# Kernel optimization log

Measured on AMD Instinct MI355X. Metric: run time of the kernel, lower is better.

## Reference

```python
import jax, jax.numpy as jnp
import numpy as np

M, N, D_MODEL = 16, 2048, 512
H, D = 8, 64  # num_heads, head_dim; inner_dim = H*D = 512


def setup_inputs() -> dict:
    key = jax.random.key(0)
    ks = jax.random.split(key, 8)
    s = 1.0 / np.sqrt(D_MODEL)
    return {
        "xq": jax.random.normal(ks[0], (M, N, D_MODEL), jnp.float32),
        "xk": jax.random.normal(ks[1], (M, N, D_MODEL), jnp.float32),
        "xv": jax.random.normal(ks[2], (M, N, D_MODEL), jnp.float32),
        "Wq": jax.random.normal(ks[3], (D_MODEL, H * D), jnp.float32) * s,
        "Wk": jax.random.normal(ks[4], (D_MODEL, H * D), jnp.float32) * s,
        "Wv": jax.random.normal(ks[5], (D_MODEL, H * D), jnp.float32) * s,
        "Wo": jax.random.normal(ks[6], (H * D, D_MODEL), jnp.float32) * s,
        "bo": jnp.zeros((D_MODEL,), jnp.float32),
    }


def _split_heads(x):
    # [m, n, h*d] -> [m, h, n, d]
    m, n, _ = x.shape
    return x.reshape(m, n, H, D).transpose(0, 2, 1, 3)


def reference(xq, xk, xv, Wq, Wk, Wv, Wo, bo):
    scale = D ** -0.5
    q = _split_heads(xq @ Wq)
    k = _split_heads(xk @ Wk)
    v = _split_heads(xv @ Wv)
    # linear attention: softmax over feature dim for both q and k
    q = jax.nn.softmax(q, axis=-1) * scale
    k = jax.nn.softmax(k, axis=-1)
    kv = jnp.einsum('mhnd,mhne->mhde', k, v)   # [m, h, d, d]
    out = jnp.einsum('mhqd,mhde->mhqe', q, kv)  # [m, h, nq, d]
    out = out.transpose(0, 2, 1, 3).reshape(out.shape[0], -1, H * D)
    return out @ Wo + bo
```

## Files before the change

kernel.cpp:

```cpp
#include <hip/hip_runtime.h>
#include <hip/hip_bf16.h>


typedef __bf16 bf16;
typedef __bf16 bf16x8 __attribute__((ext_vector_type(8)));
typedef __bf16 bf16x4 __attribute__((ext_vector_type(4)));
typedef float  f32x4  __attribute__((ext_vector_type(4)));

#define MFMA16(a, b, c) __builtin_amdgcn_mfma_f32_16x16x32_bf16((a), (b), (c), 0, 0, 0)

__device__ inline bf16x8 cvt8(float4 a, float4 b) {
  bf16x8 h;
  h[0] = (bf16)a.x; h[1] = (bf16)a.y; h[2] = (bf16)a.z; h[3] = (bf16)a.w;
  h[4] = (bf16)b.x; h[5] = (bf16)b.y; h[6] = (bf16)b.z; h[7] = (bf16)b.w;
  return h;
}

__global__ __launch_bounds__(256) void k_prep_frag(const float* __restrict__ w0, const float* __restrict__ w1,
                                                   const float* __restrict__ w2,
                                                   bf16* __restrict__ f0, bf16* __restrict__ f1,
                                                   bf16* __restrict__ f2)
{
  const float* W = (blockIdx.z == 0) ? w0 : (blockIdx.z == 1) ? w1 : w2;
  bf16*        F = (blockIdx.z == 0) ? f0 : (blockIdx.z == 1) ? f1 : f2;
  __shared__ float lds[64][68];
  const int t = threadIdx.x;
  const int bx = blockIdx.x, by = blockIdx.y;
  {
    const int r = t >> 2, c0 = (t & 3) << 4;
    const float* src = W + (size_t)(bx * 64 + r) * 512 + by * 64 + c0;
    float4 a = ((const float4*)src)[0], b = ((const float4*)src)[1];
    float4 c = ((const float4*)src)[2], d = ((const float4*)src)[3];
    *(float4*)&lds[r][c0 + 0]  = a; *(float4*)&lds[r][c0 + 4]  = b;
    *(float4*)&lds[r][c0 + 8]  = c; *(float4*)&lds[r][c0 + 12] = d;
  }
  __syncthreads();
#pragma unroll
  for (int it = 0; it < 2; ++it) {
    const int ch = t + it * 256;
    const int kc = ch >> 6, cc = ch & 63;
    bf16x8 v;
#pragma unroll
    for (int j = 0; j < 8; ++j) v[j] = (bf16)lds[kc * 8 + j][cc];
    const int cg   = by >> 1;
    const int cb7  = ((by & 1) << 2) | (cc >> 4);
    const int ksub = kc >> 2, g = kc & 3, li = cc & 15;
    const size_t off = (size_t)cg * 65536 + (size_t)bx * 8192 + ksub * 4096 + cb7 * 512 + (g * 16 + li) * 8;
    *(bf16x8*)(F + off) = v;
  }
}

__global__ __launch_bounds__(256) void k_prep_wo(const float* __restrict__ W, bf16* __restrict__ T)
{
  __shared__ float lds[64][68];
  const int t = threadIdx.x;
  const int r = t >> 2, c0 = (t & 3) << 4;
  const float* src = W + (size_t)(blockIdx.x * 64 + r) * 512 + blockIdx.y * 64 + c0;
  float4 f0 = ((const float4*)src)[0];
  float4 f1 = ((const float4*)src)[1];
  float4 f2 = ((const float4*)src)[2];
  float4 f3 = ((const float4*)src)[3];
  *(float4*)&lds[r][c0 + 0]  = f0;
  *(float4*)&lds[r][c0 + 4]  = f1;
  *(float4*)&lds[r][c0 + 8]  = f2;
  *(float4*)&lds[r][c0 + 12] = f3;
  __syncthreads();
  bf16 v[16];
#pragma unroll
  for (int s = 0; s < 16; ++s) v[s] = (bf16)lds[c0 + s][r];
  bf16* dst = T + (size_t)(blockIdx.y * 64 + r) * 512 + blockIdx.x * 64 + c0;
  *(bf16x8*)&dst[0] = *(bf16x8*)&v[0];
  *(bf16x8*)&dst[8] = *(bf16x8*)&v[8];
}

__global__ __launch_bounds__(512, 2) void k_qkv(const float* __restrict__ xq, const float* __restrict__ xk,
                                                const float* __restrict__ xv,
                                                const bf16* __restrict__ Fq, const bf16* __restrict__ Fk,
                                                const bf16* __restrict__ Fv,
                                                bf16* __restrict__ Qo, bf16* __restrict__ Ko,
                                                bf16* __restrict__ Vo)
{
  const int proj = blockIdx.z;
  const float* X  = (proj == 0) ? xq : (proj == 1) ? xk : xv;
  const bf16*  F  = (proj == 0) ? Fq : (proj == 1) ? Fk : Fv;
  bf16*       OUT = (proj == 0) ? Qo : (proj == 1) ? Ko : Vo;

  __shared__ bf16 As[2][128][72];

  const int t = threadIdx.x, lane = t & 63, w = t >> 6;
  const int g = lane >> 4, li = lane & 15;
  const size_t arow = (size_t)blockIdx.x * 128;

  const bf16* Fw = F + (w >> 1) * 65536 + (w & 1) * 2048 + lane * 8;

  const int sr = t >> 2, sc = (t & 3) << 4;
  const float* xp0 = X + (arow + sr) * 512 + sc;

  f32x4 acc[8][4] = {};

  {
    float4 xa[4];
#pragma unroll
    for (int i = 0; i < 4; ++i) xa[i] = ((const float4*)xp0)[i];
    *(bf16x8*)&As[0][sr][sc]     = cvt8(xa[0], xa[1]);
    *(bf16x8*)&As[0][sr][sc + 8] = cvt8(xa[2], xa[3]);
  }
  bf16x8 bfc[4];
#pragma unroll
  for (int ct = 0; ct < 4; ++ct) bfc[ct] = *(const bf16x8*)(Fw + ct * 512);
  __syncthreads();

  float4 xa[4];
#pragma unroll
  for (int hs = 0; hs < 16; ++hs) {
    const int kt = hs >> 1, cur = kt & 1;
    bf16x8 bfn[4];
    if (hs < 15) {
      const bf16* p = Fw + ((hs + 1) >> 1) * 8192 + ((hs + 1) & 1) * 4096;
#pragma unroll
      for (int ct = 0; ct < 4; ++ct) bfn[ct] = *(const bf16x8*)(p + ct * 512);
    }
    if ((hs & 1) == 0 && kt < 7) {
#pragma unroll
      for (int i = 0; i < 4; ++i) xa[i] = ((const float4*)(xp0 + (kt + 1) * 64))[i];
    }
    {
      bf16x8 af[8];
#pragma unroll
      for (int rt = 0; rt < 8; ++rt)
        af[rt] = *(const bf16x8*)&As[cur][rt * 16 + li][(hs & 1) * 32 + g * 8];
#pragma unroll
      for (int rt = 0; rt < 8; ++rt)
#pragma unroll
        for (int ct = 0; ct < 4; ++ct)
          acc[rt][ct] = MFMA16(af[rt], bfc[ct], acc[rt][ct]);
    }
    if (hs & 1) {
      if (kt < 7) {
        *(bf16x8*)&As[cur ^ 1][sr][sc]     = cvt8(xa[0], xa[1]);
        *(bf16x8*)&As[cur ^ 1][sr][sc + 8] = cvt8(xa[2], xa[3]);
      }
      if (hs < 15) __syncthreads();
    }
    if (hs < 15) {
#pragma unroll
      for (int ct = 0; ct < 4; ++ct) bfc[ct] = bfn[ct];
    }
  }

#pragma unroll
  for (int rt = 0; rt < 8; ++rt) {
#pragma unroll
    for (int q = 0; q < 4; ++q) {
      float v0 = acc[rt][0][q], v1 = acc[rt][1][q], v2 = acc[rt][2][q], v3 = acc[rt][3][q];
      if (proj < 2) {
        float mx = fmaxf(fmaxf(v0, v1), fmaxf(v2, v3));
        mx = fmaxf(mx, __shfl_xor(mx, 1));
        mx = fmaxf(mx, __shfl_xor(mx, 2));
        mx = fmaxf(mx, __shfl_xor(mx, 4));
        mx = fmaxf(mx, __shfl_xor(mx, 8));
        v0 = __expf(v0 - mx); v1 = __expf(v1 - mx); v2 = __expf(v2 - mx); v3 = __expf(v3 - mx);
        float s = v0 + v1 + v2 + v3;
        s += __shfl_xor(s, 1); s += __shfl_xor(s, 2); s += __shfl_xor(s, 4); s += __shfl_xor(s, 8);
        const float inv = (proj == 0 ? 0.125f : 1.0f) / s;
        v0 *= inv; v1 *= inv; v2 *= inv; v3 *= inv;
      }
      bf16* o = OUT + (arow + rt * 16 + g * 4 + q) * 512 + w * 64 + li;
      o[0] = (bf16)v0; o[16] = (bf16)v1; o[32] = (bf16)v2; o[48] = (bf16)v3;
    }
  }
}

__global__ __launch_bounds__(256) void k_kv(const bf16* __restrict__ K, const bf16* __restrict__ V,
                                            float* __restrict__ kvp)
{
  const int mh = blockIdx.x, m = mh >> 3, h = mh & 7;
  const int ns = blockIdx.y;
  __shared__ bf16 Kt[64][40];
  __shared__ bf16 Vt[64][40];
  const int t = threadIdx.x, lane = t & 63, wave = t >> 6;
  const int dq = wave >> 1, eq = wave & 1;
  const int g = lane >> 4, li = lane & 15;
  const int tn = t & 31, d0 = (t >> 5) << 3;
  const size_t rowbase = (size_t)m * 2048 + ns * 512;

  f32x4 acc[2][2] = {};

  for (int nt = 0; nt < 16; ++nt) {
    __syncthreads();
    {
      bf16x8 kr = *(const bf16x8*)(K + (rowbase + nt * 32 + tn) * 512 + h * 64 + d0);
      bf16x8 vr = *(const bf16x8*)(V + (rowbase + nt * 32 + tn) * 512 + h * 64 + d0);
#pragma unroll
      for (int j = 0; j < 8; ++j) Kt[d0 + j][tn] = kr[j];
#pragma unroll
      for (int j = 0; j < 8; ++j) Vt[d0 + j][tn] = vr[j];
    }
    __syncthreads();
    bf16x8 af[2], bfr[2];
#pragma unroll
    for (int dt = 0; dt < 2; ++dt) af[dt]  = *(const bf16x8*)&Kt[dq * 32 + dt * 16 + li][g * 8];
#pragma unroll
    for (int et = 0; et < 2; ++et) bfr[et] = *(const bf16x8*)&Vt[eq * 32 + et * 16 + li][g * 8];
#pragma unroll
    for (int dt = 0; dt < 2; ++dt)
#pragma unroll
      for (int et = 0; et < 2; ++et)
        acc[dt][et] = MFMA16(af[dt], bfr[et], acc[dt][et]);
  }

  float* o = kvp + ((size_t)mh * 4 + ns) * 4096;
#pragma unroll
  for (int dt = 0; dt < 2; ++dt)
#pragma unroll
    for (int et = 0; et < 2; ++et)
#pragma unroll
      for (int q = 0; q < 4; ++q) {
        const int d = dq * 32 + dt * 16 + g * 4 + q;
        const int e = eq * 32 + et * 16 + li;
        o[d * 64 + e] = acc[dt][et][q];
      }
}

__global__ __launch_bounds__(512) void k_wfused(const float* __restrict__ kvp, const bf16* __restrict__ WoT,
                                                bf16* __restrict__ WfT)
{
  const int mh = blockIdx.x, m = mh >> 3, h = mh & 7;
  __shared__ bf16 kvs[64][72];
  const int t = threadIdx.x, lane = t & 63, wave = t >> 6;
  const int g = lane >> 4, li = lane & 15;
  {
    const int d = t >> 3, e0 = (t & 7) << 3;
    const float* p = kvp + (size_t)mh * 16384 + d * 64 + e0;
#pragma unroll
    for (int j = 0; j < 8; ++j) {
      float s = p[j] + p[4096 + j] + p[8192 + j] + p[12288 + j];
      kvs[d][e0 + j] = (bf16)s;
    }
  }
  __syncthreads();
  f32x4 acc[4][4] = {};
#pragma unroll
  for (int kk = 0; kk < 2; ++kk) {
    bf16x8 af[4], bfr[4];
#pragma unroll
    for (int rt = 0; rt < 4; ++rt) {
      const int c = wave * 64 + rt * 16 + li;
      af[rt] = *(const bf16x8*)(WoT + (size_t)c * 512 + h * 64 + kk * 32 + g * 8);
    }
#pragma unroll
    for (int ct = 0; ct < 4; ++ct)
      bfr[ct] = *(const bf16x8*)&kvs[ct * 16 + li][kk * 32 + g * 8];
#pragma unroll
    for (int rt = 0; rt < 4; ++rt)
#pragma unroll
      for (int ct = 0; ct < 4; ++ct)
        acc[rt][ct] = MFMA16(af[rt], bfr[ct], acc[rt][ct]);
  }
  bf16* o = WfT + (size_t)m * 262144;
#pragma unroll
  for (int rt = 0; rt < 4; ++rt)
#pragma unroll
    for (int ct = 0; ct < 4; ++ct)
#pragma unroll
      for (int q = 0; q < 4; ++q) {
        const int c = wave * 64 + rt * 16 + g * 4 + q;
        const int r = h * 64 + ct * 16 + li;
        o[(size_t)c * 512 + r] = (bf16)acc[rt][ct][q];
      }
}

__global__ __launch_bounds__(512) void k_out(const bf16* __restrict__ Q, const bf16* __restrict__ WfT,
                                             const float* __restrict__ bo, float* __restrict__ out)
{
  __shared__ bf16 As2[64][40];
  __shared__ bf16 Bs[512][40];
  const int rb = blockIdx.x;
  const int m = rb >> 5;
  const bf16* B = WfT + (size_t)m * 262144;
  const int t = threadIdx.x, lane = t & 63, wave = t >> 6;
  const int g = lane >> 4, li = lane & 15;
  const size_t arow = (size_t)rb * 64;

  f32x4 acc[4][4] = {};
  const int ar = t >> 3, ac = (t & 7) << 2;
  const int br = t >> 2, bc = (t & 3) << 3;

  for (int kt = 0; kt < 16; ++kt) {
    const int k0 = kt * 32;
    __syncthreads();
    {
      bf16x4 a = *(const bf16x4*)(Q + (arow + ar) * 512 + k0 + ac);
      *(bf16x4*)&As2[ar][ac] = a;
    }
#pragma unroll
    for (int i = 0; i < 4; ++i) {
      const int r = br + i * 128;
      bf16x8 b = *(const bf16x8*)(B + (size_t)r * 512 + k0 + bc);
      *(bf16x8*)&Bs[r][bc] = b;
    }
    __syncthreads();
    bf16x8 af[4], bfr[4];
#pragma unroll
    for (int rt = 0; rt < 4; ++rt) af[rt]  = *(const bf16x8*)&As2[rt * 16 + li][g * 8];
#pragma unroll
    for (int ct = 0; ct < 4; ++ct) bfr[ct] = *(const bf16x8*)&Bs[wave * 64 + ct * 16 + li][g * 8];
#pragma unroll
    for (int rt = 0; rt < 4; ++rt)
#pragma unroll
      for (int ct = 0; ct < 4; ++ct)
        acc[rt][ct] = MFMA16(af[rt], bfr[ct], acc[rt][ct]);
  }

  float bv[4];
#pragma unroll
  for (int ct = 0; ct < 4; ++ct) bv[ct] = bo[wave * 64 + ct * 16 + li];
#pragma unroll
  for (int rt = 0; rt < 4; ++rt)
#pragma unroll
    for (int q = 0; q < 4; ++q) {
      float* o = out + (arow + rt * 16 + g * 4 + q) * 512 + wave * 64 + li;
      o[0]  = acc[rt][0][q] + bv[0];
      o[16] = acc[rt][1][q] + bv[1];
      o[32] = acc[rt][2][q] + bv[2];
      o[48] = acc[rt][3][q] + bv[3];
    }
}

extern "C" void kernel_launch(void* const* d_in, const int* in_sizes, int n_in,
                              void* d_out, int out_size, void* d_ws, size_t ws_size,
                              hipStream_t stream)
{
  const float* xq = (const float*)d_in[0];
  const float* xk = (const float*)d_in[1];
  const float* xv = (const float*)d_in[2];
  const float* Wq = (const float*)d_in[3];
  const float* Wk = (const float*)d_in[4];
  const float* Wv = (const float*)d_in[5];
  const float* Wo = (const float*)d_in[6];
  const float* bo = (const float*)d_in[7];
  float* out = (float*)d_out;

  char* ws = (char*)d_ws;
  const size_t WT_BYTES  = 512 * 512 * 2;
  const size_t QKV_BYTES = (size_t)32768 * 512 * 2;
  bf16*  WFq = (bf16*)(ws);
  bf16*  WFk = (bf16*)(ws + WT_BYTES);
  bf16*  WFv = (bf16*)(ws + 2 * WT_BYTES);
  bf16*  WoT = (bf16*)(ws + 3 * WT_BYTES);
  bf16*  Qb  = (bf16*)(ws + 4 * WT_BYTES);
  bf16*  Kb  = (bf16*)(ws + 4 * WT_BYTES + QKV_BYTES);
  bf16*  Vb  = (bf16*)(ws + 4 * WT_BYTES + 2 * QKV_BYTES);
  float* kvp = (float*)(ws + 4 * WT_BYTES + 3 * QKV_BYTES);
  bf16*  WfT = Kb;

  k_prep_frag<<<dim3(8, 8, 3), 256, 0, stream>>>(Wq, Wk, Wv, WFq, WFk, WFv);
  k_prep_wo  <<<dim3(8, 8),    256, 0, stream>>>(Wo, WoT);
  k_qkv      <<<dim3(256, 1, 3), 512, 0, stream>>>(xq, xk, xv, WFq, WFk, WFv, Qb, Kb, Vb);
  k_kv       <<<dim3(128, 4),  256, 0, stream>>>(Kb, Vb, kvp);
  k_wfused   <<<dim3(128),     512, 0, stream>>>(kvp, WoT, WfT);
  k_out      <<<dim3(512),     512, 0, stream>>>(Qb, WfT, bo, out);
}
```

Measured before the change: 178.2 us.

## Drop LDS staging in QKV and output GEMMs, read MFMA fragments directly

The QKV projection kernel now uses 64-row tiles with a flat 1536-block grid and no LDS double buffering. Each lane loads and converts its A fragment straight from global fp32 memory, and occupancy is raised to 4 blocks per CU. The fused-weight kernel now writes its output in a pre-swizzled MFMA fragment layout, so the output GEMM can load B fragments directly from global memory without LDS or barriers. This removes shared-memory traffic and syncs but gives up cross-wave reuse of A tiles, which means more redundant global and L2 reads.

```diff
diff --git a/kernel.cpp b/kernel.cpp
--- a/kernel.cpp
+++ b/kernel.cpp
@@ -73,83 +73,51 @@
   *(bf16x8*)&dst[8] = *(bf16x8*)&v[8];
 }
 
-__global__ __launch_bounds__(512, 2) void k_qkv(const float* __restrict__ xq, const float* __restrict__ xk,
+__global__ __launch_bounds__(512, 4) void k_qkv(const float* __restrict__ xq, const float* __restrict__ xk,
                                                 const float* __restrict__ xv,
                                                 const bf16* __restrict__ Fq, const bf16* __restrict__ Fk,
                                                 const bf16* __restrict__ Fv,
                                                 bf16* __restrict__ Qo, bf16* __restrict__ Ko,
                                                 bf16* __restrict__ Vo)
 {
-  const int proj = blockIdx.z;
+  const int b = blockIdx.x;
+  const int proj = b >> 9;
+  const int rb   = b & 511;
   const float* X  = (proj == 0) ? xq : (proj == 1) ? xk : xv;
   const bf16*  F  = (proj == 0) ? Fq : (proj == 1) ? Fk : Fv;
   bf16*       OUT = (proj == 0) ? Qo : (proj == 1) ? Ko : Vo;
 
-  __shared__ bf16 As[2][128][72];
-
   const int t = threadIdx.x, lane = t & 63, w = t >> 6;
   const int g = lane >> 4, li = lane & 15;
-  const size_t arow = (size_t)blockIdx.x * 128;
-
-  const bf16* Fw = F + (w >> 1) * 65536 + (w & 1) * 2048 + lane * 8;
-
-  const int sr = t >> 2, sc = (t & 3) << 4;
-  const float* xp0 = X + (arow + sr) * 512 + sc;
-
-  f32x4 acc[8][4] = {};
-
-  {
-    float4 xa[4];
-#pragma unroll
-    for (int i = 0; i < 4; ++i) xa[i] = ((const float4*)xp0)[i];
-    *(bf16x8*)&As[0][sr][sc]     = cvt8(xa[0], xa[1]);
-    *(bf16x8*)&As[0][sr][sc + 8] = cvt8(xa[2], xa[3]);
-  }
-  bf16x8 bfc[4];
-#pragma unroll
-  for (int ct = 0; ct < 4; ++ct) bfc[ct] = *(const bf16x8*)(Fw + ct * 512);
-  __syncthreads();
-
-  float4 xa[4];
-#pragma unroll
-  for (int hs = 0; hs < 16; ++hs) {
-    const int kt = hs >> 1, cur = kt & 1;
-    bf16x8 bfn[4];
-    if (hs < 15) {
-      const bf16* p = Fw + ((hs + 1) >> 1) * 8192 + ((hs + 1) & 1) * 4096;
-#pragma unroll
-      for (int ct = 0; ct < 4; ++ct) bfn[ct] = *(const bf16x8*)(p + ct * 512);
-    }
-    if ((hs & 1) == 0 && kt < 7) {
-#pragma unroll
-      for (int i = 0; i < 4; ++i) xa[i] = ((const float4*)(xp0 + (kt + 1) * 64))[i];
-    }
-    {
-      bf16x8 af[8];
-#pragma unroll
-      for (int rt = 0; rt < 8; ++rt)
-        af[rt] = *(const bf16x8*)&As[cur][rt * 16 + li][(hs & 1) * 32 + g * 8];
-#pragma unroll
-      for (int rt = 0; rt < 8; ++rt)
-#pragma unroll
-        for (int ct = 0; ct < 4; ++ct)
-          acc[rt][ct] = MFMA16(af[rt], bfc[ct], acc[rt][ct]);
-    }
-    if (hs & 1) {
-      if (kt < 7) {
-        *(bf16x8*)&As[cur ^ 1][sr][sc]     = cvt8(xa[0], xa[1]);
-        *(bf16x8*)&As[cur ^ 1][sr][sc + 8] = cvt8(xa[2], xa[3]);
-      }
-      if (hs < 15) __syncthreads();
-    }
-    if (hs < 15) {
-#pragma unroll
-      for (int ct = 0; ct < 4; ++ct) bfc[ct] = bfn[ct];
-    }
-  }
-
-#pragma unroll
-  for (int rt = 0; rt < 8; ++rt) {
+  const size_t arow = (size_t)rb * 64;
+
+  const float* ap = X + (arow + li) * 512 + g * 8;
+  const bf16*  bp = F + (w >> 1) * 65536 + (w & 1) * 2048 + lane * 8;
+
+  f32x4 acc[4][4] = {};
+
+#pragma unroll 4
+  for (int kt = 0; kt < 16; ++kt) {
+    bf16x8 af[4], bfr[4];
+#pragma unroll
+    for (int rt = 0; rt < 4; ++rt) {
+      const float* p = ap + rt * 8192 + kt * 32;
+      float4 f0 = ((const float4*)p)[0];
+      float4 f1 = ((const float4*)p)[1];
+      af[rt] = cvt8(f0, f1);
+    }
+#pragma unroll
+    for (int ct = 0; ct < 4; ++ct)
+      bfr[ct] = *(const bf16x8*)(bp + kt * 4096 + ct * 512);
+#pragma unroll
+    for (int rt = 0; rt < 4; ++rt)
+#pragma unroll
+      for (int ct = 0; ct < 4; ++ct)
+        acc[rt][ct] = MFMA16(af[rt], bfr[ct], acc[rt][ct]);
+  }
+
+#pragma unroll
+  for (int rt = 0; rt < 4; ++rt) {
 #pragma unroll
     for (int q = 0; q < 4; ++q) {
       float v0 = acc[rt][0][q], v1 = acc[rt][1][q], v2 = acc[rt][2][q], v3 = acc[rt][3][q];
@@ -223,11 +191,11 @@
 }
 
 __global__ __launch_bounds__(512) void k_wfused(const float* __restrict__ kvp, const bf16* __restrict__ WoT,
-                                                bf16* __restrict__ WfT)
+                                                bf16* __restrict__ WfF)
 {
   const int mh = blockIdx.x, m = mh >> 3, h = mh & 7;
   __shared__ bf16 kvs[64][72];
-  const int t = threadIdx.x, lane = t & 63, wave = t >> 6;
+  const int t = threadIdx.x, lane = t & 63, wv = t >> 6;
   const int g = lane >> 4, li = lane & 15;
   {
     const int d = t >> 3, e0 = (t & 7) << 3;
@@ -242,84 +210,77 @@
   f32x4 acc[4][4] = {};
 #pragma unroll
   for (int kk = 0; kk < 2; ++kk) {
+    bf16x8 a_kv[4], b_wo[4];
+#pragma unroll
+    for (int rt = 0; rt < 4; ++rt)
+      a_kv[rt] = *(const bf16x8*)&kvs[rt * 16 + li][kk * 32 + g * 8];
+#pragma unroll
+    for (int ct = 0; ct < 4; ++ct) {
+      const int cout = wv * 64 + ct * 16 + li;
+      b_wo[ct] = *(const bf16x8*)(WoT + (size_t)cout * 512 + h * 64 + kk * 32 + g * 8);
+    }
+#pragma unroll
+    for (int rt = 0; rt < 4; ++rt)
+#pragma unroll
+      for (int ct = 0; ct < 4; ++ct)
+        acc[rt][ct] = MFMA16(a_kv[rt], b_wo[ct], acc[rt][ct]);
+  }
+  bf16* o = WfF + (size_t)m * 262144;
+#pragma unroll
+  for (int rt = 0; rt < 4; ++rt)
+#pragma unroll
+    for (int ct = 0; ct < 4; ++ct) {
+      const int cgct  = wv * 4 + ct;
+      const int cg    = cgct >> 3, cb7 = cgct & 7;
+      const int lane2 = ((rt & 1) * 2 + (g >> 1)) * 16 + li;
+      const size_t off = (size_t)cg * 65536 + (size_t)h * 8192 + (rt >> 1) * 4096
+                       + cb7 * 512 + lane2 * 8 + (g & 1) * 4;
+      bf16x4 v;
+#pragma unroll
+      for (int q = 0; q < 4; ++q) v[q] = (bf16)acc[rt][ct][q];
+      *(bf16x4*)(o + off) = v;
+    }
+}
+
+__global__ __launch_bounds__(512, 4) void k_out(const bf16* __restrict__ Q, const bf16* __restrict__ WfF,
+                                                const float* __restrict__ bo, float* __restrict__ out)
+{
+  const int rb = blockIdx.x;
+  const int m  = rb >> 5;
+  const bf16* Fm = WfF + (size_t)m * 262144;
+  const int t = threadIdx.x, lane = t & 63, w = t >> 6;
+  const int g = lane >> 4, li = lane & 15;
+  const size_t arow = (size_t)rb * 64;
+
+  const bf16* apq = Q + (arow + li) * 512 + g * 8;
+  const bf16* bp  = Fm + (w >> 1) * 65536 + (w & 1) * 2048 + lane * 8;
+
+  f32x4 acc[4][4] = {};
+
+#pragma unroll 4
+  for (int kt = 0; kt < 16; ++kt) {
     bf16x8 af[4], bfr[4];
 #pragma unroll
-    for (int rt = 0; rt < 4; ++rt) {
-      const int c = wave * 64 + rt * 16 + li;
-      af[rt] = *(const bf16x8*)(WoT + (size_t)c * 512 + h * 64 + kk * 32 + g * 8);
-    }
+    for (int rt = 0; rt < 4; ++rt)
+      af[rt] = *(const bf16x8*)(apq + rt * 8192 + kt * 32);
 #pragma unroll
     for (int ct = 0; ct < 4; ++ct)
-      bfr[ct] = *(const bf16x8*)&kvs[ct * 16 + li][kk * 32 + g * 8];
+      bfr[ct] = *(const bf16x8*)(bp + kt * 4096 + ct * 512);
 #pragma unroll
     for (int rt = 0; rt < 4; ++rt)
 #pragma unroll
       for (int ct = 0; ct < 4; ++ct)
         acc[rt][ct] = MFMA16(af[rt], bfr[ct], acc[rt][ct]);
   }
-  bf16* o = WfT + (size_t)m * 262144;
+
+  float bv[4];
+#pragma unroll
+  for (int ct = 0; ct < 4; ++ct) bv[ct] = bo[w * 64 + ct * 16 + li];
 #pragma unroll
   for (int rt = 0; rt < 4; ++rt)
 #pragma unroll
-    for (int ct = 0; ct < 4; ++ct)
-#pragma unroll
-      for (int q = 0; q < 4; ++q) {
-        const int c = wave * 64 + rt * 16 + g * 4 + q;
-        const int r = h * 64 + ct * 16 + li;
-        o[(size_t)c * 512 + r] = (bf16)acc[rt][ct][q];
-      }
-}
-
-__global__ __launch_bounds__(512) void k_out(const bf16* __restrict__ Q, const bf16* __restrict__ WfT,
-                                             const float* __restrict__ bo, float* __restrict__ out)
-{
-  __shared__ bf16 As2[64][40];
-  __shared__ bf16 Bs[512][40];
-  const int rb = blockIdx.x;
-  const int m = rb >> 5;
-  const bf16* B = WfT + (size_t)m * 262144;
-  const int t = threadIdx.x, lane = t & 63, wave = t >> 6;
-  const int g = lane >> 4, li = lane & 15;
-  const size_t arow = (size_t)rb * 64;
-
-  f32x4 acc[4][4] = {};
-  const int ar = t >> 3, ac = (t & 7) << 2;
-  const int br = t >> 2, bc = (t & 3) << 3;
-
-  for (int kt = 0; kt < 16; ++kt) {
-    const int k0 = kt * 32;
-    __syncthreads();
-    {
-      bf16x4 a = *(const bf16x4*)(Q + (arow + ar) * 512 + k0 + ac);
-      *(bf16x4*)&As2[ar][ac] = a;
-    }
-#pragma unroll
-    for (int i = 0; i < 4; ++i) {
-      const int r = br + i * 128;
-      bf16x8 b = *(const bf16x8*)(B + (size_t)r * 512 + k0 + bc);
-      *(bf16x8*)&Bs[r][bc] = b;
-    }
-    __syncthreads();
-    bf16x8 af[4], bfr[4];
-#pragma unroll
-    for (int rt = 0; rt < 4; ++rt) af[rt]  = *(const bf16x8*)&As2[rt * 16 + li][g * 8];
-#pragma unroll
-    for (int ct = 0; ct < 4; ++ct) bfr[ct] = *(const bf16x8*)&Bs[wave * 64 + ct * 16 + li][g * 8];
-#pragma unroll
-    for (int rt = 0; rt < 4; ++rt)
-#pragma unroll
-      for (int ct = 0; ct < 4; ++ct)
-        acc[rt][ct] = MFMA16(af[rt], bfr[ct], acc[rt][ct]);
-  }
-
-  float bv[4];
-#pragma unroll
-  for (int ct = 0; ct < 4; ++ct) bv[ct] = bo[wave * 64 + ct * 16 + li];
-#pragma unroll
-  for (int rt = 0; rt < 4; ++rt)
-#pragma unroll
     for (int q = 0; q < 4; ++q) {
-      float* o = out + (arow + rt * 16 + g * 4 + q) * 512 + wave * 64 + li;
+      float* o = out + (arow + rt * 16 + g * 4 + q) * 512 + w * 64 + li;
       o[0]  = acc[rt][0][q] + bv[0];
       o[16] = acc[rt][1][q] + bv[1];
       o[32] = acc[rt][2][q] + bv[2];
@@ -352,12 +313,12 @@
   bf16*  Kb  = (bf16*)(ws + 4 * WT_BYTES + QKV_BYTES);
   bf16*  Vb  = (bf16*)(ws + 4 * WT_BYTES + 2 * QKV_BYTES);
   float* kvp = (float*)(ws + 4 * WT_BYTES + 3 * QKV_BYTES);
-  bf16*  WfT = Kb;
+  bf16*  WfF = Kb;
 
   k_prep_frag<<<dim3(8, 8, 3), 256, 0, stream>>>(Wq, Wk, Wv, WFq, WFk, WFv);
   k_prep_wo  <<<dim3(8, 8),    256, 0, stream>>>(Wo, WoT);
-  k_qkv      <<<dim3(256, 1, 3), 512, 0, stream>>>(xq, xk, xv, WFq, WFk, WFv, Qb, Kb, Vb);
+  k_qkv      <<<dim3(1536),    512, 0, stream>>>(xq, xk, xv, WFq, WFk, WFv, Qb, Kb, Vb);
   k_kv       <<<dim3(128, 4),  256, 0, stream>>>(Kb, Vb, kvp);
-  k_wfused   <<<dim3(128),     512, 0, stream>>>(kvp, WoT, WfT);
-  k_out      <<<dim3(512),     512, 0, stream>>>(Qb, WfT, bo, out);
-}
+  k_wfused   <<<dim3(128),     512, 0, stream>>>(kvp, WoT, WfF);
+  k_out      <<<dim3(512),     512, 0, stream>>>(Qb, WfF, bo, out);
+}
```

Measured after the change: 310.7 us. 1.74x slower.
